# Optimization experiments

Hardware: AMD Instinct MI355X
Metric: run time of the kernel (lower is better)

Reference implementation:

```python
import jax, jax.numpy as jnp
import numpy as np
import math

D_MODEL = 1024
NUM_HEADS = 16
D_K = D_MODEL // NUM_HEADS
B, S = 2, 2048


def setup_inputs() -> dict:
    key = jax.random.key(0)
    ks = jax.random.split(key, 11)
    scale = 1.0 / math.sqrt(D_MODEL)
    inp = {
        "query": jax.random.normal(ks[0], (B, S, D_MODEL), jnp.float32),
        "key": jax.random.normal(ks[1], (B, S, D_MODEL), jnp.float32),
        "value": jax.random.normal(ks[2], (B, S, D_MODEL), jnp.float32),
        "Wq": jax.random.normal(ks[3], (D_MODEL, D_MODEL), jnp.float32) * scale,
        "bq": jnp.zeros((D_MODEL,), jnp.float32),
        "Wk": jax.random.normal(ks[4], (D_MODEL, D_MODEL), jnp.float32) * scale,
        "bk": jnp.zeros((D_MODEL,), jnp.float32),
        "Wv": jax.random.normal(ks[5], (D_MODEL, D_MODEL), jnp.float32) * scale,
        "bv": jnp.zeros((D_MODEL,), jnp.float32),
        "Wo": jax.random.normal(ks[6], (D_MODEL, D_MODEL), jnp.float32) * scale,
        "bo": jnp.zeros((D_MODEL,), jnp.float32),
    }
    return inp


def reference(query, key, value, Wq, bq, Wk, bk, Wv, bv, Wo, bo):
    b, s, _ = query.shape
    # QKV projections (torch Linear: x @ W.T + b)
    Q = query @ Wq.T + bq
    K = key @ Wk.T + bk
    V = value @ Wv.T + bv
    # [b, h, s, d_k]
    Q = Q.reshape(b, s, NUM_HEADS, D_K).transpose(0, 2, 1, 3)
    K = K.reshape(b, s, NUM_HEADS, D_K).transpose(0, 2, 1, 3)
    V = V.reshape(b, s, NUM_HEADS, D_K).transpose(0, 2, 1, 3)
    score = jnp.einsum("bhqd,bhkd->bhqk", Q, K) / math.sqrt(D_K)
    attn = jax.nn.softmax(score, axis=-1)
    out = jnp.einsum("bhqk,bhkd->bhqd", attn, V)
    out = out.transpose(0, 2, 1, 3).reshape(b, s, D_MODEL)
    return out @ Wo.T + bo
```

## Files before the change

### kernel.cpp

```cpp
#include <hip/hip_runtime.h>

#define NHEADS 16
#define SEQ    2048
#define BATCH  2
#define DMODEL 1024
#define MTOT   4096

typedef __attribute__((ext_vector_type(8)))  short short8;
typedef __attribute__((ext_vector_type(4)))  float f32x4;
typedef __attribute__((ext_vector_type(16))) float f32x16;

__device__ __forceinline__ unsigned short f32_to_bf16_rn(float x) {
  unsigned int u = __float_as_uint(x);
  u += 0x7fffu + ((u >> 16) & 1u);
  return (unsigned short)(u >> 16);
}

__device__ __forceinline__ unsigned cvt_pk_bf16(float lo, float hi_) {
  unsigned r;
  asm("v_cvt_pk_bf16_f32 %0, %1, %2" : "=v"(r) : "v"(lo), "v"(hi_));
  return r;
}

__device__ __forceinline__ void permlane32_swap(unsigned &a, unsigned &b) {
  asm("v_permlane32_swap_b32 %0, %1" : "+v"(a), "+v"(b));
}

__device__ __forceinline__ void async16(void* lds, const void* g) {
  __builtin_amdgcn_global_load_lds((const __attribute__((address_space(1))) unsigned int*)g,
                                   (__attribute__((address_space(3))) unsigned int*)lds, 16, 0, 0);
}

__global__ void cvt_bf16_kernel(const float* __restrict__ x0, const float* __restrict__ x1,
                                const float* __restrict__ x2,
                                const float* __restrict__ w0, const float* __restrict__ w1,
                                const float* __restrict__ w2, const float* __restrict__ w3,
                                unsigned short* __restrict__ obase)
{
  const int e = (blockIdx.x*256 + threadIdx.x)*8;
  const float* src;
  int local;
  if (e < 3*4194304) {
    const int t = e >> 22;
    src = t==0 ? x0 : t==1 ? x1 : x2;
    local = e & (4194304-1);
    src += local;
    local += t << 22;
  } else {
    const int f = e - 3*4194304;
    const int t = f >> 20;
    src = t==0 ? w0 : t==1 ? w1 : t==2 ? w2 : w3;
    src += (f & (1048576-1));
    local = e;
  }
  const float4 v0 = *(const float4*)(src);
  const float4 v1 = *(const float4*)(src + 4);
  union { unsigned short u[8]; uint4 v; } r;
  r.u[0] = f32_to_bf16_rn(v0.x); r.u[1] = f32_to_bf16_rn(v0.y);
  r.u[2] = f32_to_bf16_rn(v0.z); r.u[3] = f32_to_bf16_rn(v0.w);
  r.u[4] = f32_to_bf16_rn(v1.x); r.u[5] = f32_to_bf16_rn(v1.y);
  r.u[6] = f32_to_bf16_rn(v1.z); r.u[7] = f32_to_bf16_rn(v1.w);
  *(uint4*)(obase + local) = r.v;
}

template<int BM>
__device__ __forceinline__ void gemm_core(const unsigned short* __restrict__ A,
                                          const unsigned short* __restrict__ W,
                                          unsigned short* sA, unsigned short* sB,
                                          int m0, int n0, f32x4 (&acc)[BM/32][4])
{
  constexpr int MI = BM/32;
  const int t = threadIdx.x;
  const int lane = t & 63;
  const int wv = t >> 6;
  const int wm = wv >> 1, wn = wv & 1;
  const int lr = lane & 15, lk = lane >> 4;

  for (int kt = 0; kt < DMODEL/64; ++kt) {
    #pragma unroll
    for (int g = 0; g < MI; ++g) {
      const int o  = g*4096 + t*16;
      const int so = o ^ (((o >> 7) & 7) << 4);
      const int row = so >> 7, colE = (so & 127) >> 1;
      async16((char*)sA + o, A + (size_t)(m0 + row)*DMODEL + kt*64 + colE);
    }
    #pragma unroll
    for (int g = 0; g < 4; ++g) {
      const int o  = g*4096 + t*16;
      const int so = o ^ (((o >> 7) & 7) << 4);
      const int row = so >> 7, colE = (so & 127) >> 1;
      async16((char*)sB + o, W + (size_t)(n0 + row)*DMODEL + kt*64 + colE);
    }
    __syncthreads();
    #pragma unroll
    for (int ks = 0; ks < 2; ++ks) {
      short8 af[MI], bf[4];
      #pragma unroll
      for (int mi = 0; mi < MI; ++mi) {
        const int row = wm*(BM/2) + mi*16 + lr;
        const int sl  = (ks*4 + lk) ^ (row & 7);
        af[mi] = *(const short8*)(sA + row*64 + sl*8);
      }
      #pragma unroll
      for (int ni = 0; ni < 4; ++ni) {
        const int row = wn*64 + ni*16 + lr;
        const int sl  = (ks*4 + lk) ^ (row & 7);
        bf[ni] = *(const short8*)(sB + row*64 + sl*8);
      }
      #pragma unroll
      for (int mi = 0; mi < MI; ++mi)
        #pragma unroll
        for (int ni = 0; ni < 4; ++ni)
          acc[mi][ni] = __builtin_amdgcn_mfma_f32_16x16x32_bf16(af[mi], bf[ni], acc[mi][ni], 0, 0, 0);
    }
    __syncthreads();
  }
}

__global__ __launch_bounds__(256, 2)
void qkv_gemm_kernel(const unsigned short* __restrict__ Xq, const unsigned short* __restrict__ Xk,
                     const unsigned short* __restrict__ Xv,
                     const unsigned short* __restrict__ Wq, const unsigned short* __restrict__ Wk,
                     const unsigned short* __restrict__ Wv,
                     const float* __restrict__ bq, const float* __restrict__ bk,
                     const float* __restrict__ bv,
                     unsigned short* __restrict__ Qp, unsigned short* __restrict__ Kp,
                     unsigned short* __restrict__ Vtp)
{
  constexpr int BM = 128;
  constexpr int MI = BM/32;
  __shared__ __align__(16) unsigned short sA[BM*64];
  __shared__ __align__(16) unsigned short sB[128*64];

  const int m0   = blockIdx.x * BM;
  const int nabs = blockIdx.y * 128;
  const int wsel = nabs >> 10;
  const int n0   = nabs & 1023;
  const unsigned short* A = wsel==0 ? Xq : wsel==1 ? Xk : Xv;
  const unsigned short* W = wsel==0 ? Wq : wsel==1 ? Wk : Wv;
  const float* bias       = wsel==0 ? bq : wsel==1 ? bk : bv;
  unsigned short* dst     = wsel==0 ? Qp : wsel==1 ? Kp : Vtp;

  f32x4 acc[MI][4];
  #pragma unroll
  for (int mi = 0; mi < MI; ++mi)
    #pragma unroll
    for (int ni = 0; ni < 4; ++ni)
      acc[mi][ni] = {0.f, 0.f, 0.f, 0.f};

  gemm_core<BM>(A, W, sA, sB, m0, n0, acc);

  const int t = threadIdx.x, lane = t & 63, wvx = t >> 6;
  const int wm = wvx >> 1, wn = wvx & 1;
  const int lr = lane & 15, lk = lane >> 4;
  const float qscale = (wsel == 0) ? 0.125f * 1.4426950408889634f : 1.0f;

  #pragma unroll
  for (int ni = 0; ni < 4; ++ni) {
    const int nn = n0 + wn*64 + ni*16 + lr;
    const float badd = bias[nn];
    const int hh = nn >> 6, d = nn & 63;
    #pragma unroll
    for (int mi = 0; mi < MI; ++mi) {
      #pragma unroll
      for (int r = 0; r < 4; ++r) {
        const int m = m0 + wm*(BM/2) + mi*16 + lk*4 + r;
        const int bb = m >> 11, s = m & 2047;
        const float v = (acc[mi][ni][r] + badd) * qscale;
        size_t idx;
        if (wsel == 2) idx = (((size_t)bb*NHEADS + hh)*64 + d)*SEQ + s;
        else           idx = (((size_t)bb*NHEADS + hh)*SEQ + s)*64 + d;
        dst[idx] = f32_to_bf16_rn(v);
      }
    }
  }
}

__global__ __launch_bounds__(256, 2)
void attn_kernel(const unsigned short* __restrict__ Qp, const unsigned short* __restrict__ Kp,
                 const unsigned short* __restrict__ Vtp, unsigned short* __restrict__ Op)
{
  __shared__ __align__(16) unsigned short sm[16384];

  const int t = threadIdx.x, lane = t & 63, w = t >> 6;
  const int lq = lane & 31, hi = lane >> 5;
  const int qt = blockIdx.x, h = blockIdx.y, b = blockIdx.z;
  const size_t bh = (size_t)b*NHEADS + h;
  const unsigned short* Qh = Qp  + bh*SEQ*64;
  const unsigned short* Kh = Kp  + bh*SEQ*64;
  const unsigned short* Vh = Vtp + bh*64*SEQ;
  const int q0 = qt*128 + w*32;

  short8 qf[4];
  #pragma unroll
  for (int ks = 0; ks < 4; ++ks)
    qf[ks] = *(const short8*)(Qh + (size_t)(q0 + lq)*64 + ks*16 + hi*8);

  union { unsigned u[4]; short8 s; } ones;
  #pragma unroll
  for (int i = 0; i < 4; ++i) ones.u[i] = 0x3F803F80u;

  const unsigned short* srcp;
  size_t sstride;
  if (w < 2) { srcp = Kh + (size_t)(w*32 + lq)*64 + hi*8;        sstride = 64*64; }
  else       { srcp = Vh + (size_t)((w-2)*32 + lq)*2048 + hi*8;  sstride = 64;    }

  #pragma unroll
  for (int i = 0; i < 4; ++i)
    async16((char*)sm + w*4096 + i*1024, srcp + i*16);
  srcp += sstride;
  asm volatile("s_waitcnt vmcnt(0)" ::: "memory");
  __syncthreads();

  f32x16 o[2], ls;
  #pragma unroll
  for (int d = 0; d < 2; ++d)
    #pragma unroll
    for (int r = 0; r < 16; ++r) o[d][r] = 0.f;
  #pragma unroll
  for (int r = 0; r < 16; ++r) ls[r] = 0.f;

  #pragma unroll 2
  for (int kt = 0; kt < SEQ/64; ++kt) {
    if (kt + 1 < SEQ/64) {
      const int nb = ((kt + 1) & 1) * 16384;
      #pragma unroll
      for (int i = 0; i < 4; ++i)
        async16((char*)sm + nb + w*4096 + i*1024, srcp + i*16);
      srcp += sstride;
    }
    const unsigned short* base  = sm + (kt & 1)*8192;
    const unsigned short* vbase = base + 4096;

    f32x16 st[2];
    #pragma unroll
    for (int s = 0; s < 2; ++s)
      #pragma unroll
      for (int r = 0; r < 16; ++r) st[s][r] = 0.f;
    __builtin_amdgcn_s_setprio(1);
    #pragma unroll
    for (int sub = 0; sub < 2; ++sub)
      #pragma unroll
      for (int ks = 0; ks < 4; ++ks) {
        const short8 kf = *(const short8*)(base + (sub*4 + ks)*512 + lane*8);
        st[sub] = __builtin_amdgcn_mfma_f32_32x32x16_bf16(kf, qf[ks], st[sub], 0, 0, 0);
      }
    __builtin_amdgcn_s_setprio(0);

    #pragma unroll
    for (int s = 0; s < 2; ++s)
      #pragma unroll
      for (int r = 0; r < 16; ++r)
        st[s][r] = __builtin_amdgcn_exp2f(st[s][r]);

    #pragma unroll
    for (int sub = 0; sub < 2; ++sub) {
      union { unsigned u[4]; short8 s; } pA, pB;
      {
        unsigned x0 = cvt_pk_bf16(st[sub][0],  st[sub][1]);
        unsigned x1 = cvt_pk_bf16(st[sub][2],  st[sub][3]);
        unsigned y0 = cvt_pk_bf16(st[sub][4],  st[sub][5]);
        unsigned y1 = cvt_pk_bf16(st[sub][6],  st[sub][7]);
        permlane32_swap(x0, y0);
        permlane32_swap(x1, y1);
        pA.u[0] = x0; pA.u[1] = x1; pA.u[2] = y0; pA.u[3] = y1;
        unsigned z0 = cvt_pk_bf16(st[sub][8],  st[sub][9]);
        unsigned z1 = cvt_pk_bf16(st[sub][10], st[sub][11]);
        unsigned w0 = cvt_pk_bf16(st[sub][12], st[sub][13]);
        unsigned w1 = cvt_pk_bf16(st[sub][14], st[sub][15]);
        permlane32_swap(z0, w0);
        permlane32_swap(z1, w1);
        pB.u[0] = z0; pB.u[1] = z1; pB.u[2] = w0; pB.u[3] = w1;
      }
      const short8 v00 = *(const short8*)(vbase + (0*4 + 2*sub    )*512 + lane*8);
      const short8 v01 = *(const short8*)(vbase + (0*4 + 2*sub + 1)*512 + lane*8);
      const short8 v10 = *(const short8*)(vbase + (1*4 + 2*sub    )*512 + lane*8);
      const short8 v11 = *(const short8*)(vbase + (1*4 + 2*sub + 1)*512 + lane*8);
      __builtin_amdgcn_s_setprio(1);
      o[0] = __builtin_amdgcn_mfma_f32_32x32x16_bf16(v00, pA.s, o[0], 0, 0, 0);
      o[1] = __builtin_amdgcn_mfma_f32_32x32x16_bf16(v10, pA.s, o[1], 0, 0, 0);
      ls   = __builtin_amdgcn_mfma_f32_32x32x16_bf16(ones.s, pA.s, ls, 0, 0, 0);
      o[0] = __builtin_amdgcn_mfma_f32_32x32x16_bf16(v01, pB.s, o[0], 0, 0, 0);
      o[1] = __builtin_amdgcn_mfma_f32_32x32x16_bf16(v11, pB.s, o[1], 0, 0, 0);
      ls   = __builtin_amdgcn_mfma_f32_32x32x16_bf16(ones.s, pB.s, ls, 0, 0, 0);
      __builtin_amdgcn_s_setprio(0);
    }
    asm volatile("s_waitcnt vmcnt(0)" ::: "memory");
    __syncthreads();
  }

  const float inv = __builtin_amdgcn_rcpf(ls[0]);
  unsigned short* orow = Op + ((size_t)b*SEQ + q0 + lq)*DMODEL + h*64;
  #pragma unroll
  for (int dblk = 0; dblk < 2; ++dblk)
    #pragma unroll
    for (int g = 0; g < 4; ++g) {
      union { unsigned short us[4]; uint2 v; } pk;
      #pragma unroll
      for (int r = 0; r < 4; ++r) pk.us[r] = f32_to_bf16_rn(o[dblk][g*4 + r] * inv);
      *(uint2*)(orow + dblk*32 + g*8 + hi*4) = pk.v;
    }
}

__global__ __launch_bounds__(256, 2)
void oproj_gemm_kernel(const unsigned short* __restrict__ Oin, const unsigned short* __restrict__ Wo,
                       const float* __restrict__ bo, float* __restrict__ out)
{
  constexpr int BM = 64;
  constexpr int MI = BM/32;
  __shared__ __align__(16) unsigned short sA[BM*64];
  __shared__ __align__(16) unsigned short sB[128*64];
  const int m0 = blockIdx.x * BM;
  const int n0 = blockIdx.y * 128;

  f32x4 acc[MI][4];
  #pragma unroll
  for (int mi = 0; mi < MI; ++mi)
    #pragma unroll
    for (int ni = 0; ni < 4; ++ni)
      acc[mi][ni] = {0.f,0.f,0.f,0.f};

  gemm_core<BM>(Oin, Wo, sA, sB, m0, n0, acc);

  const int t = threadIdx.x, lane = t & 63, wvx = t >> 6;
  const int wm = wvx >> 1, wn = wvx & 1;
  const int lr = lane & 15, lk = lane >> 4;

  #pragma unroll
  for (int ni = 0; ni < 4; ++ni) {
    const int nn = n0 + wn*64 + ni*16 + lr;
    const float badd = bo[nn];
    #pragma unroll
    for (int mi = 0; mi < MI; ++mi)
      #pragma unroll
      for (int r = 0; r < 4; ++r) {
        const int m = m0 + wm*(BM/2) + mi*16 + lk*4 + r;
        out[(size_t)m*DMODEL + nn] = acc[mi][ni][r] + badd;
      }
  }
}

extern "C" void kernel_launch(void* const* d_in, const int* in_sizes, int n_in,
                              void* d_out, int out_size, void* d_ws, size_t ws_size,
                              hipStream_t stream) {
  const float* query = (const float*)d_in[0];
  const float* key   = (const float*)d_in[1];
  const float* value = (const float*)d_in[2];
  const float* Wq    = (const float*)d_in[3];
  const float* bq    = (const float*)d_in[4];
  const float* Wk    = (const float*)d_in[5];
  const float* bk    = (const float*)d_in[6];
  const float* Wv    = (const float*)d_in[7];
  const float* bv    = (const float*)d_in[8];
  const float* Wo    = (const float*)d_in[9];
  const float* bo    = (const float*)d_in[10];

  const size_t NX = (size_t)MTOT*DMODEL;
  const size_t NW = (size_t)DMODEL*DMODEL;
  unsigned short* w   = (unsigned short*)d_ws;
  unsigned short* Xq  = w;
  unsigned short* Xk  = Xq  + NX;
  unsigned short* Xv  = Xk  + NX;
  unsigned short* Wqp = Xv  + NX;
  unsigned short* Wkp = Wqp + NW;
  unsigned short* Wvp = Wkp + NW;
  unsigned short* Wop = Wvp + NW;
  unsigned short* Qp  = Wop + NW;
  unsigned short* Kp  = Qp  + NX;
  unsigned short* Vtp = Kp  + NX;
  unsigned short* Opb = Vtp + NX;

  cvt_bf16_kernel<<<dim3(8192), 256, 0, stream>>>(
      query, key, value, Wq, Wk, Wv, Wo, w);
  qkv_gemm_kernel<<<dim3(32, 24), 256, 0, stream>>>(
      Xq, Xk, Xv, Wqp, Wkp, Wvp, bq, bk, bv, Qp, Kp, Vtp);
  attn_kernel<<<dim3(16, 16, 2), 256, 0, stream>>>(Qp, Kp, Vtp, Opb);
  oproj_gemm_kernel<<<dim3(64, 8), 256, 0, stream>>>(Opb, Wop, bo, (float*)d_out);
}
```

Baseline: 118.0 us.

## Triple-buffer attention K/V tiles, software-pipeline QK^T, stage V-transpose stores via LDS

The attention kernel moves from double to triple-buffered LDS tiles and computes the next tile's QK^T MFMAs before the current tile's exp/PV work, so tensor-core and transcendental work can overlap. It also remaps block indices so neighbouring blocks spread across heads and batches. The QKV GEMM epilogue for V now writes the transposed tile into shared memory and issues coalesced 16-byte stores instead of scattered 2-byte writes. The cost is more LDS per block and more live accumulator registers, which could lower occupancy.

```diff
diff --git a/kernel.cpp b/kernel.cpp
--- a/kernel.cpp
+++ b/kernel.cpp
@@ -129,8 +129,9 @@
 {
   constexpr int BM = 128;
   constexpr int MI = BM/32;
-  __shared__ __align__(16) unsigned short sA[BM*64];
-  __shared__ __align__(16) unsigned short sB[128*64];
+  __shared__ __align__(16) unsigned short smem[17024];
+  unsigned short* sA = smem;
+  unsigned short* sB = smem + 8192;
 
   const int m0   = blockIdx.x * BM;
   const int nabs = blockIdx.y * 128;
@@ -139,7 +140,6 @@
   const unsigned short* A = wsel==0 ? Xq : wsel==1 ? Xk : Xv;
   const unsigned short* W = wsel==0 ? Wq : wsel==1 ? Wk : Wv;
   const float* bias       = wsel==0 ? bq : wsel==1 ? bk : bv;
-  unsigned short* dst     = wsel==0 ? Qp : wsel==1 ? Kp : Vtp;
 
   f32x4 acc[MI][4];
   #pragma unroll
@@ -153,24 +153,46 @@
   const int t = threadIdx.x, lane = t & 63, wvx = t >> 6;
   const int wm = wvx >> 1, wn = wvx & 1;
   const int lr = lane & 15, lk = lane >> 4;
-  const float qscale = (wsel == 0) ? 0.125f * 1.4426950408889634f : 1.0f;
-
-  #pragma unroll
-  for (int ni = 0; ni < 4; ++ni) {
-    const int nn = n0 + wn*64 + ni*16 + lr;
-    const float badd = bias[nn];
-    const int hh = nn >> 6, d = nn & 63;
-    #pragma unroll
-    for (int mi = 0; mi < MI; ++mi) {
-      #pragma unroll
-      for (int r = 0; r < 4; ++r) {
-        const int m = m0 + wm*(BM/2) + mi*16 + lk*4 + r;
-        const int bb = m >> 11, s = m & 2047;
-        const float v = (acc[mi][ni][r] + badd) * qscale;
-        size_t idx;
-        if (wsel == 2) idx = (((size_t)bb*NHEADS + hh)*64 + d)*SEQ + s;
-        else           idx = (((size_t)bb*NHEADS + hh)*SEQ + s)*64 + d;
-        dst[idx] = f32_to_bf16_rn(v);
+
+  if (wsel == 2) {
+    #pragma unroll
+    for (int ni = 0; ni < 4; ++ni) {
+      const float badd = bias[n0 + wn*64 + ni*16 + lr];
+      #pragma unroll
+      for (int mi = 0; mi < MI; ++mi)
+        #pragma unroll
+        for (int r = 0; r < 4; ++r) {
+          const int ml = wm*(BM/2) + mi*16 + lk*4 + r;
+          smem[(wn*64 + ni*16 + lr)*132 + ml] = f32_to_bf16_rn(acc[mi][ni][r] + badd);
+        }
+    }
+    __syncthreads();
+    const int bb = m0 >> 11, s0 = m0 & 2047;
+    const int jr = (t & 15)*8, nr = t >> 4;
+    #pragma unroll
+    for (int pass = 0; pass < 8; ++pass) {
+      const int n  = pass*16 + nr;
+      const int nn = n0 + n, hh = nn >> 6, d = nn & 63;
+      const short8 v = *(const short8*)(smem + n*132 + jr);
+      *(short8*)(Vtp + (((size_t)bb*NHEADS + hh)*64 + d)*SEQ + s0 + jr) = v;
+    }
+  } else {
+    unsigned short* dst = wsel==0 ? Qp : Kp;
+    const float qscale = (wsel == 0) ? 0.125f * 1.4426950408889634f : 1.0f;
+    #pragma unroll
+    for (int ni = 0; ni < 4; ++ni) {
+      const int nn = n0 + wn*64 + ni*16 + lr;
+      const float badd = bias[nn];
+      const int hh = nn >> 6, d = nn & 63;
+      #pragma unroll
+      for (int mi = 0; mi < MI; ++mi) {
+        #pragma unroll
+        for (int r = 0; r < 4; ++r) {
+          const int m = m0 + wm*(BM/2) + mi*16 + lk*4 + r;
+          const int bb = m >> 11, s = m & 2047;
+          const float v = (acc[mi][ni][r] + badd) * qscale;
+          dst[(((size_t)bb*NHEADS + hh)*SEQ + s)*64 + d] = f32_to_bf16_rn(v);
+        }
       }
     }
   }
@@ -180,11 +202,15 @@
 void attn_kernel(const unsigned short* __restrict__ Qp, const unsigned short* __restrict__ Kp,
                  const unsigned short* __restrict__ Vtp, unsigned short* __restrict__ Op)
 {
-  __shared__ __align__(16) unsigned short sm[16384];
+  __shared__ __align__(16) unsigned short sm[3*8192];
+  constexpr int NT = SEQ/64;
 
   const int t = threadIdx.x, lane = t & 63, w = t >> 6;
   const int lq = lane & 31, hi = lane >> 5;
-  const int qt = blockIdx.x, h = blockIdx.y, b = blockIdx.z;
+  const int f   = blockIdx.x + 16*blockIdx.y + 256*blockIdx.z;
+  const int wid = (f & 7)*64 + (f >> 3);
+  const int qt = wid & 15, h = (wid >> 4) & 15, b = wid >> 8;
+
   const size_t bh = (size_t)b*NHEADS + h;
   const unsigned short* Qh = Qp  + bh*SEQ*64;
   const unsigned short* Kh = Kp  + bh*SEQ*64;
@@ -206,76 +232,86 @@
   else       { srcp = Vh + (size_t)((w-2)*32 + lq)*2048 + hi*8;  sstride = 64;    }
 
   #pragma unroll
-  for (int i = 0; i < 4; ++i)
-    async16((char*)sm + w*4096 + i*1024, srcp + i*16);
+  for (int i = 0; i < 4; ++i) async16((char*)sm + 0     + w*4096 + i*1024, srcp + i*16);
   srcp += sstride;
-  asm volatile("s_waitcnt vmcnt(0)" ::: "memory");
+  #pragma unroll
+  for (int i = 0; i < 4; ++i) async16((char*)sm + 16384 + w*4096 + i*1024, srcp + i*16);
+  srcp += sstride;
+
+  f32x16 o[2], ls, stA[2], stB[2];
+  #pragma unroll
+  for (int d = 0; d < 2; ++d)
+    #pragma unroll
+    for (int r = 0; r < 16; ++r) { o[d][r] = 0.f; stA[d][r] = 0.f; stB[d][r] = 0.f; }
+  #pragma unroll
+  for (int r = 0; r < 16; ++r) ls[r] = 0.f;
+
+  asm volatile("s_waitcnt vmcnt(4)" ::: "memory");
   __syncthreads();
-
-  f32x16 o[2], ls;
-  #pragma unroll
-  for (int d = 0; d < 2; ++d)
-    #pragma unroll
-    for (int r = 0; r < 16; ++r) o[d][r] = 0.f;
-  #pragma unroll
-  for (int r = 0; r < 16; ++r) ls[r] = 0.f;
-
-  #pragma unroll 2
-  for (int kt = 0; kt < SEQ/64; ++kt) {
-    if (kt + 1 < SEQ/64) {
-      const int nb = ((kt + 1) & 1) * 16384;
+  __builtin_amdgcn_s_setprio(1);
+  #pragma unroll
+  for (int sub = 0; sub < 2; ++sub)
+    #pragma unroll
+    for (int ks = 0; ks < 4; ++ks) {
+      const short8 kf = *(const short8*)(sm + (sub*4 + ks)*512 + lane*8);
+      stA[sub] = __builtin_amdgcn_mfma_f32_32x32x16_bf16(kf, qf[ks], stA[sub], 0, 0, 0);
+    }
+  __builtin_amdgcn_s_setprio(0);
+
+  auto body = [&](f32x16 (&cur)[2], f32x16 (&nxt)[2], int tc, int obC, int obN, int obS) {
+    asm volatile("s_waitcnt vmcnt(0)" ::: "memory");
+    __syncthreads();
+    if (tc + 2 < NT) {
       #pragma unroll
       for (int i = 0; i < 4; ++i)
-        async16((char*)sm + nb + w*4096 + i*1024, srcp + i*16);
+        async16((char*)sm + obS + w*4096 + i*1024, srcp + i*16);
       srcp += sstride;
     }
-    const unsigned short* base  = sm + (kt & 1)*8192;
-    const unsigned short* vbase = base + 4096;
-
-    f32x16 st[2];
+    if (tc + 1 < NT) {
+      const unsigned short* kb = sm + (obN >> 1);
+      #pragma unroll
+      for (int s = 0; s < 2; ++s)
+        #pragma unroll
+        for (int r = 0; r < 16; ++r) nxt[s][r] = 0.f;
+      __builtin_amdgcn_s_setprio(1);
+      #pragma unroll
+      for (int sub = 0; sub < 2; ++sub)
+        #pragma unroll
+        for (int ks = 0; ks < 4; ++ks) {
+          const short8 kf = *(const short8*)(kb + (sub*4 + ks)*512 + lane*8);
+          nxt[sub] = __builtin_amdgcn_mfma_f32_32x32x16_bf16(kf, qf[ks], nxt[sub], 0, 0, 0);
+        }
+      __builtin_amdgcn_s_setprio(0);
+    }
     #pragma unroll
     for (int s = 0; s < 2; ++s)
       #pragma unroll
-      for (int r = 0; r < 16; ++r) st[s][r] = 0.f;
-    __builtin_amdgcn_s_setprio(1);
-    #pragma unroll
-    for (int sub = 0; sub < 2; ++sub)
-      #pragma unroll
-      for (int ks = 0; ks < 4; ++ks) {
-        const short8 kf = *(const short8*)(base + (sub*4 + ks)*512 + lane*8);
-        st[sub] = __builtin_amdgcn_mfma_f32_32x32x16_bf16(kf, qf[ks], st[sub], 0, 0, 0);
-      }
-    __builtin_amdgcn_s_setprio(0);
-
-    #pragma unroll
-    for (int s = 0; s < 2; ++s)
-      #pragma unroll
       for (int r = 0; r < 16; ++r)
-        st[s][r] = __builtin_amdgcn_exp2f(st[s][r]);
-
+        cur[s][r] = __builtin_amdgcn_exp2f(cur[s][r]);
+    const unsigned short* vb = sm + (obC >> 1) + 4096;
     #pragma unroll
     for (int sub = 0; sub < 2; ++sub) {
       union { unsigned u[4]; short8 s; } pA, pB;
       {
-        unsigned x0 = cvt_pk_bf16(st[sub][0],  st[sub][1]);
-        unsigned x1 = cvt_pk_bf16(st[sub][2],  st[sub][3]);
-        unsigned y0 = cvt_pk_bf16(st[sub][4],  st[sub][5]);
-        unsigned y1 = cvt_pk_bf16(st[sub][6],  st[sub][7]);
+        unsigned x0 = cvt_pk_bf16(cur[sub][0],  cur[sub][1]);
+        unsigned x1 = cvt_pk_bf16(cur[sub][2],  cur[sub][3]);
+        unsigned y0 = cvt_pk_bf16(cur[sub][4],  cur[sub][5]);
+        unsigned y1 = cvt_pk_bf16(cur[sub][6],  cur[sub][7]);
         permlane32_swap(x0, y0);
         permlane32_swap(x1, y1);
         pA.u[0] = x0; pA.u[1] = x1; pA.u[2] = y0; pA.u[3] = y1;
-        unsigned z0 = cvt_pk_bf16(st[sub][8],  st[sub][9]);
-        unsigned z1 = cvt_pk_bf16(st[sub][10], st[sub][11]);
-        unsigned w0 = cvt_pk_bf16(st[sub][12], st[sub][13]);
-        unsigned w1 = cvt_pk_bf16(st[sub][14], st[sub][15]);
+        unsigned z0 = cvt_pk_bf16(cur[sub][8],  cur[sub][9]);
+        unsigned z1 = cvt_pk_bf16(cur[sub][10], cur[sub][11]);
+        unsigned w0 = cvt_pk_bf16(cur[sub][12], cur[sub][13]);
+        unsigned w1 = cvt_pk_bf16(cur[sub][14], cur[sub][15]);
         permlane32_swap(z0, w0);
         permlane32_swap(z1, w1);
         pB.u[0] = z0; pB.u[1] = z1; pB.u[2] = w0; pB.u[3] = w1;
       }
-      const short8 v00 = *(const short8*)(vbase + (0*4 + 2*sub    )*512 + lane*8);
-      const short8 v01 = *(const short8*)(vbase + (0*4 + 2*sub + 1)*512 + lane*8);
-      const short8 v10 = *(const short8*)(vbase + (1*4 + 2*sub    )*512 + lane*8);
-      const short8 v11 = *(const short8*)(vbase + (1*4 + 2*sub + 1)*512 + lane*8);
+      const short8 v00 = *(const short8*)(vb + (0*4 + 2*sub    )*512 + lane*8);
+      const short8 v01 = *(const short8*)(vb + (0*4 + 2*sub + 1)*512 + lane*8);
+      const short8 v10 = *(const short8*)(vb + (1*4 + 2*sub    )*512 + lane*8);
+      const short8 v11 = *(const short8*)(vb + (1*4 + 2*sub + 1)*512 + lane*8);
       __builtin_amdgcn_s_setprio(1);
       o[0] = __builtin_amdgcn_mfma_f32_32x32x16_bf16(v00, pA.s, o[0], 0, 0, 0);
       o[1] = __builtin_amdgcn_mfma_f32_32x32x16_bf16(v10, pA.s, o[1], 0, 0, 0);
@@ -285,8 +321,14 @@
       ls   = __builtin_amdgcn_mfma_f32_32x32x16_bf16(ones.s, pB.s, ls, 0, 0, 0);
       __builtin_amdgcn_s_setprio(0);
     }
-    asm volatile("s_waitcnt vmcnt(0)" ::: "memory");
-    __syncthreads();
+  };
+
+  int obC = 0, obN = 16384, obS = 32768;
+  for (int t2 = 0; t2 < NT; t2 += 2) {
+    body(stA, stB, t2,     obC, obN, obS);
+    int tmp = obC; obC = obN; obN = obS; obS = tmp;
+    body(stB, stA, t2 + 1, obC, obN, obS);
+    tmp = obC; obC = obN; obN = obS; obS = tmp;
   }
 
   const float inv = __builtin_amdgcn_rcpf(ls[0]);
```

New measurement: 113.0 us. 4.3% less time.
